# Kernel optimization log

Hardware: AMD Instinct MI355X
Metric: run time of the kernel (lower is better)

Reference implementation:

```python
import jax, jax.numpy as jnp
import numpy as np

N_NODES = 500_000
N_EDGES = 4_000_000


def setup_inputs() -> dict:
    key = jax.random.key(0)
    k1, k2, k3, k4 = jax.random.split(key, 4)
    x = jax.random.normal(k1, (N_NODES, 3), dtype=jnp.float32)
    edge_index = jax.random.randint(k2, (2, N_EDGES), 0, N_NODES, dtype=jnp.int32)
    # GCNConv(3, 16) and GCNConv(16, 1): weight [in, out], bias [out]
    W1 = jax.random.normal(k3, (3, 16), dtype=jnp.float32) / np.sqrt(3.0)
    b1 = jnp.zeros((16,), dtype=jnp.float32)
    W2 = jax.random.normal(k4, (16, 1), dtype=jnp.float32) / np.sqrt(16.0)
    b2 = jnp.zeros((1,), dtype=jnp.float32)
    return {"x": x, "edge_index": edge_index, "W1": W1, "b1": b1, "W2": W2, "b2": b2}


def gcn_conv(x, edge_index, W, b):
    """PyG GCNConv: add self-loops, symmetric deg^-1/2 normalization,
    linear transform, scatter-add aggregation to target nodes, bias."""
    n = x.shape[0]
    loop = jnp.arange(n, dtype=edge_index.dtype)
    row = jnp.concatenate([edge_index[0], loop])  # source nodes
    col = jnp.concatenate([edge_index[1], loop])  # target nodes
    deg = jax.ops.segment_sum(jnp.ones_like(col, dtype=x.dtype), col, num_segments=n)
    deg_inv_sqrt = jnp.where(deg > 0, jax.lax.rsqrt(jnp.maximum(deg, 1.0)), 0.0)
    norm = deg_inv_sqrt[row] * deg_inv_sqrt[col]  # [E+N]
    h = x @ W  # [N, out]
    msg = h[row] * norm[:, None]  # gather + scale, [E+N, out]
    out = jax.ops.segment_sum(msg, col, num_segments=n)  # scatter-add
    return out + b


def reference(x, edge_index, W1, b1, W2, b2):
    h = jax.nn.relu(gcn_conv(x, edge_index, W1, b1))
    return gcn_conv(h, edge_index, W2, b2)  # [N, 1]
```

## Files before the change

### kernel.cpp

```cpp
#include <hip/hip_runtime.h>
#include <hip/hip_fp16.h>


typedef float vf4 __attribute__((ext_vector_type(4)));

#define NB 512
#define SHIFT 10
#define SLICE 1024
#define CAP 11264
#define P1T 1024
#define P1PER 16
#define P1G 256
#define SENT 0xFFFFFFFFu

__global__ __launch_bounds__(1024) void p1_partition(
        const int* __restrict__ row, const int* __restrict__ col,
        unsigned* __restrict__ gcur, unsigned* __restrict__ buf, int E) {
    __shared__ unsigned hist[NB];
    __shared__ unsigned loff[NB], lcur[NB], gbase[NB], bcnt[NB];
    __shared__ unsigned stage[P1T * P1PER];
    __shared__ unsigned wsum[16];
    int t = threadIdx.x;
    if (t < NB) hist[t] = 0;
    __syncthreads();
    int per = (E + P1G - 1) / P1G;
    per = (per + 3) & ~3;
    long long base = (long long)blockIdx.x * per;
    long long eend = base + per; if (eend > E) eend = E;
    int nch = (per + 4095) / 4096;
    unsigned ent[P1PER];
    int bkt[P1PER];
#pragma unroll
    for (int ch = 0; ch < 4; ch++) {
        if (ch < nch) {
            long long e = base + (long long)ch * 4096 + 4 * t;
            if (e + 3 < eend) {
                int4 c4 = *(const int4*)(col + e);
                int4 r4 = *(const int4*)(row + e);
                int cs[4] = {c4.x, c4.y, c4.z, c4.w};
                int rs[4] = {r4.x, r4.y, r4.z, r4.w};
#pragma unroll
                for (int u = 0; u < 4; u++) {
                    int j = ch * 4 + u;
                    ent[j] = ((unsigned)rs[u] << SHIFT) | (unsigned)(cs[u] & (SLICE - 1));
                    bkt[j] = cs[u] >> SHIFT;
                    atomicAdd(&hist[bkt[j]], 1u);
                }
            } else {
#pragma unroll
                for (int u = 0; u < 4; u++) {
                    int j = ch * 4 + u;
                    long long ee = e + u;
                    if (ee < eend) {
                        int c = col[ee], r = row[ee];
                        ent[j] = ((unsigned)r << SHIFT) | (unsigned)(c & (SLICE - 1));
                        bkt[j] = c >> SHIFT;
                        atomicAdd(&hist[bkt[j]], 1u);
                    } else bkt[j] = -1;
                }
            }
        } else {
#pragma unroll
            for (int u = 0; u < 4; u++) bkt[ch * 4 + u] = -1;
        }
    }
    __syncthreads();
    unsigned myc = 0, v = 0;
    int lane = t & 63, w = t >> 6;
    if (t < NB) {
        myc = hist[t];
        v = myc;
#pragma unroll
        for (int d = 1; d < 64; d <<= 1) {
            unsigned o = __shfl_up(v, d, 64);
            if (lane >= d) v += o;
        }
        if (lane == 63) wsum[w] = v;
    }
    __syncthreads();
    if (w == 0) {
        unsigned s = (lane < 8) ? wsum[lane] : 0u, sv = s;
#pragma unroll
        for (int d = 1; d < 8; d <<= 1) {
            unsigned o = __shfl_up(sv, d, 64);
            if (lane >= d) sv += o;
        }
        if (lane < 8) wsum[lane] = sv - s;
    }
    __syncthreads();
    if (t < NB) {
        unsigned excl = v - myc + wsum[w];
        loff[t] = excl;
        lcur[t] = excl;
        bcnt[t] = myc;
        unsigned padded = (myc + 3u) & ~3u;
        gbase[t] = padded ? atomicAdd(&gcur[t], padded) : 0u;
        hist[t] = padded;
    }
    __syncthreads();
#pragma unroll
    for (int j = 0; j < P1PER; j++) {
        if (bkt[j] >= 0) {
            unsigned p = atomicAdd(&lcur[bkt[j]], 1u);
            stage[p] = ent[j];
        }
    }
    __syncthreads();
    for (int bb = 0; bb < 32; bb++) {
        int bk = (w << 5) + bb;
        unsigned c = bcnt[bk], padded = hist[bk];
        unsigned lo = loff[bk], gb = gbase[bk];
        unsigned* dst = buf + (size_t)bk * CAP + gb;
        for (unsigned s = lane; s < padded; s += 64) {
            unsigned val = (s < c) ? stage[lo + s] : SENT;
            if (gb + s < CAP) dst[s] = val;
        }
    }
}

__global__ __launch_bounds__(1024, 8) void k2a1(
        const unsigned* __restrict__ gcur, const unsigned* __restrict__ buf,
        const float* __restrict__ x, uint2* __restrict__ xs4h,
        unsigned* __restrict__ pstart, int N) {
    __shared__ unsigned cnts[SLICE];
    __shared__ unsigned wsum[16];
    int b = blockIdx.x, t = threadIdx.x;
    cnts[t] = 0;
    __syncthreads();
    unsigned ext = min(gcur[b], (unsigned)CAP);
    const unsigned* bp = buf + (size_t)b * CAP;
    for (unsigned i = 4 * t; i < ext; i += 4096) {
        uint4 q = *(const uint4*)(bp + i);
        if (q.x != SENT) atomicAdd(&cnts[q.x & (SLICE - 1)], 1u);
        if (q.y != SENT) atomicAdd(&cnts[q.y & (SLICE - 1)], 1u);
        if (q.z != SENT) atomicAdd(&cnts[q.z & (SLICE - 1)], 1u);
        if (q.w != SENT) atomicAdd(&cnts[q.w & (SLICE - 1)], 1u);
    }
    __syncthreads();
    unsigned myc = cnts[t];
    unsigned pc = (myc + 3u) & ~3u;
    unsigned v = pc;
    int lane = t & 63, w = t >> 6;
#pragma unroll
    for (int d = 1; d < 64; d <<= 1) {
        unsigned o = __shfl_up(v, d, 64);
        if (lane >= d) v += o;
    }
    if (lane == 63) wsum[w] = v;
    __syncthreads();
    if (w == 0) {
        unsigned s = (lane < 16) ? wsum[lane] : 0u, sv = s;
#pragma unroll
        for (int d = 1; d < 16; d <<= 1) {
            unsigned o = __shfl_up(sv, d, 64);
            if (lane >= d) sv += o;
        }
        if (lane < 16) wsum[lane] = sv - s;
    }
    __syncthreads();
    unsigned excl = v - pc + wsum[w];
    int c = (b << SHIFT) + t;
    pstart[c] = (excl << 8) | min(myc, 255u);
    if (c < N) {
        float d = rsqrtf(1.0f + (float)myc);
        __half2 h01 = __floats2half2_rn(d * x[3 * c], d * x[3 * c + 1]);
        __half2 h23 = __floats2half2_rn(d * x[3 * c + 2], 0.f);
        uint2 u;
        u.x = *(unsigned*)&h01;
        u.y = *(unsigned*)&h23;
        xs4h[c] = u;
    }
}

__global__ __launch_bounds__(1024, 8) void k2bf(
        const unsigned* __restrict__ gcur, const unsigned* __restrict__ buf,
        const unsigned* __restrict__ pstart, const uint2* __restrict__ xs4h,
        const float* __restrict__ W1, const float* __restrict__ b1,
        const float* __restrict__ W2, unsigned* __restrict__ buf2,
        float* __restrict__ hs2, int N) {
    __shared__ __align__(16) unsigned sorted[CAP];
    __shared__ unsigned pos[SLICE];
    __shared__ unsigned stot;
    __shared__ float sW[48], sb[16], sw2[16];
    int b = blockIdx.x, t = threadIdx.x;
    if (t < 48) sW[t] = W1[t];
    if (t < 16) { sb[t] = b1[t]; sw2[t] = W2[t]; }
    unsigned meta = pstart[(b << SHIFT) + t];
    pos[t] = meta >> 8;
    if (t == SLICE - 1) {
        unsigned tt = (meta >> 8) + (((meta & 255u) + 3u) & ~3u);
        stot = min(tt, (unsigned)CAP);
    }
    __syncthreads();
    unsigned ext = min(gcur[b], (unsigned)CAP);
    const unsigned* bp = buf + (size_t)b * CAP;
    for (unsigned i = 4 * t; i < ext; i += 4096) {
        uint4 q = *(const uint4*)(bp + i);
        if (q.x != SENT) { unsigned p = atomicAdd(&pos[q.x & (SLICE - 1)], 1u); if (p < CAP) sorted[p] = q.x >> SHIFT; }
        if (q.y != SENT) { unsigned p = atomicAdd(&pos[q.y & (SLICE - 1)], 1u); if (p < CAP) sorted[p] = q.y >> SHIFT; }
        if (q.z != SENT) { unsigned p = atomicAdd(&pos[q.z & (SLICE - 1)], 1u); if (p < CAP) sorted[p] = q.z >> SHIFT; }
        if (q.w != SENT) { unsigned p = atomicAdd(&pos[q.w & (SLICE - 1)], 1u); if (p < CAP) sorted[p] = q.w >> SHIFT; }
    }
    __syncthreads();
    unsigned tot = stot;
    unsigned* b2p = buf2 + (size_t)b * CAP;
    for (unsigned i = 4 * t; i < tot; i += 4096)
        *(uint4*)(b2p + i) = *(const uint4*)(sorted + i);
    int c = (b << SHIFT) + t;
    if (c >= N) return;
    unsigned cnt = meta & 255u;
    unsigned base = meta >> 8;
    float d = rsqrtf(1.0f + (float)cnt);
    uint2 us = xs4h[c];
    float2 fs = __half22float2(*(__half2*)&us.x);
    float a0 = fs.x, a1 = fs.y, a2 = __low2float(*(__half2*)&us.y);
    unsigned j = 0;
    for (; j + 4 <= cnt; j += 4) {
        uint4 rr = *(const uint4*)(sorted + base + j);
        uint2 u0 = xs4h[rr.x], u1 = xs4h[rr.y], u2 = xs4h[rr.z], u3 = xs4h[rr.w];
        float2 f0 = __half22float2(*(__half2*)&u0.x); float g0 = __low2float(*(__half2*)&u0.y);
        float2 f1 = __half22float2(*(__half2*)&u1.x); float g1 = __low2float(*(__half2*)&u1.y);
        float2 f2 = __half22float2(*(__half2*)&u2.x); float g2 = __low2float(*(__half2*)&u2.y);
        float2 f3 = __half22float2(*(__half2*)&u3.x); float g3 = __low2float(*(__half2*)&u3.y);
        a0 += (f0.x + f1.x) + (f2.x + f3.x);
        a1 += (f0.y + f1.y) + (f2.y + f3.y);
        a2 += (g0 + g1) + (g2 + g3);
    }
    for (; j < cnt; j++) {
        uint2 u = xs4h[sorted[base + j]];
        float2 f = __half22float2(*(__half2*)&u.x);
        a0 += f.x; a1 += f.y; a2 += __low2float(*(__half2*)&u.y);
    }
    float s = 0.f;
#pragma unroll
    for (int k = 0; k < 16; k++) {
        float z = fmaxf(d * (a0 * sW[k] + a1 * sW[16 + k] + a2 * sW[32 + k]) + sb[k], 0.f);
        s += z * sw2[k];
    }
    hs2[c] = d * s;
}

__global__ __launch_bounds__(1024, 8) void k2c(
        const unsigned* __restrict__ pstart, const unsigned* __restrict__ buf2,
        const float* __restrict__ hs2, const float* __restrict__ b2,
        float* __restrict__ out, int N) {
    int b = blockIdx.x, t = threadIdx.x;
    int c = (b << SHIFT) + t;
    if (c >= N) return;
    unsigned meta = pstart[c];
    const unsigned* sp = buf2 + (size_t)b * CAP + (meta >> 8);
    unsigned cnt = meta & 255u;
    float d = rsqrtf(1.0f + (float)cnt);
    float s = hs2[c];
    unsigned j = 0;
    for (; j + 8 <= cnt; j += 8) {
        uint4 ra = *(const uint4*)(sp + j);
        uint4 rb = *(const uint4*)(sp + j + 4);
        float v0 = hs2[ra.x], v1 = hs2[ra.y], v2 = hs2[ra.z], v3 = hs2[ra.w];
        float v4 = hs2[rb.x], v5 = hs2[rb.y], v6 = hs2[rb.z], v7 = hs2[rb.w];
        s += ((v0 + v1) + (v2 + v3)) + ((v4 + v5) + (v6 + v7));
    }
    for (; j + 4 <= cnt; j += 4) {
        uint4 rr = *(const uint4*)(sp + j);
        float v0 = hs2[rr.x], v1 = hs2[rr.y], v2 = hs2[rr.z], v3 = hs2[rr.w];
        s += (v0 + v1) + (v2 + v3);
    }
    for (; j < cnt; j++) s += hs2[sp[j]];
    out[c] = d * s + b2[0];
}

__global__ void fb_deg(const int* __restrict__ col, float* __restrict__ deg, int E) {
    int e = blockIdx.x * blockDim.x + threadIdx.x;
    if (e < E) atomicAdd(&deg[col[e]], 1.0f);
}
__global__ void fb_pass_a(const float* __restrict__ x, const float* __restrict__ deg,
                          float* __restrict__ dis, vf4* __restrict__ xs4, int N) {
    int i = blockIdx.x * blockDim.x + threadIdx.x;
    if (i >= N) return;
    float d = rsqrtf(deg[i] + 1.0f);
    dis[i] = d;
    vf4 v; v.x = d * x[3 * i]; v.y = d * x[3 * i + 1]; v.z = d * x[3 * i + 2]; v.w = 0.f;
    xs4[i] = v;
}
__global__ void fb_aggx(const int* __restrict__ ei, const float* __restrict__ xs4,
                        float* __restrict__ accx, int E) {
    int t = blockIdx.x * blockDim.x + threadIdx.x;
    int e = t >> 2, k = t & 3;
    if (e >= E) return;
    int r = ei[e], c = ei[E + e];
    float val = xs4[4 * r + k];
    if (k < 3) atomicAdd(&accx[4 * c + k], val);
}
__global__ void fb_post1(const vf4* __restrict__ accx, const vf4* __restrict__ xs4,
                         const float* __restrict__ dis, const float* __restrict__ W1,
                         const float* __restrict__ b1, const float* __restrict__ W2,
                         float* __restrict__ hs2, int N) {
    __shared__ float sW[48], sb[16], sw2[16];
    if (threadIdx.x < 48) sW[threadIdx.x] = W1[threadIdx.x];
    if (threadIdx.x < 16) { sb[threadIdx.x] = b1[threadIdx.x]; sw2[threadIdx.x] = W2[threadIdx.x]; }
    __syncthreads();
    int i = blockIdx.x * blockDim.x + threadIdx.x;
    if (i >= N) return;
    vf4 a = accx[i], self = xs4[i];
    float a0 = a.x + self.x, a1 = a.y + self.y, a2 = a.z + self.z;
    float d = dis[i], s = 0.f;
#pragma unroll
    for (int k = 0; k < 16; k++) {
        float z = fmaxf(d * (a0 * sW[k] + a1 * sW[16 + k] + a2 * sW[32 + k]) + sb[k], 0.f);
        s += z * sw2[k];
    }
    hs2[i] = d * s;
}
__global__ void fb_agg2(const int* __restrict__ ei, const float* __restrict__ hs2,
                        float* __restrict__ acc2, int E) {
    int e = blockIdx.x * blockDim.x + threadIdx.x;
    if (e >= E) return;
    atomicAdd(&acc2[ei[E + e]], hs2[ei[e]]);
}
__global__ void fb_fin(const float* __restrict__ acc2, const float* __restrict__ hs2,
                       const float* __restrict__ dis, const float* __restrict__ b2,
                       float* __restrict__ out, int N) {
    int i = blockIdx.x * blockDim.x + threadIdx.x;
    if (i < N) out[i] = dis[i] * (acc2[i] + hs2[i]) + b2[0];
}

extern "C" void kernel_launch(void* const* d_in, const int* in_sizes, int n_in,
                              void* d_out, int out_size, void* d_ws, size_t ws_size,
                              hipStream_t stream) {
    const float* x  = (const float*)d_in[0];
    const int*   ei = (const int*)d_in[1];
    const float* W1 = (const float*)d_in[2];
    const float* b1 = (const float*)d_in[3];
    const float* W2 = (const float*)d_in[4];
    const float* b2 = (const float*)d_in[5];
    float* out = (float*)d_out;

    const int N = in_sizes[0] / 3;
    const int E = in_sizes[1] / 2;
    const int* row = ei;
    const int* col = ei + E;

    float* ws = (float*)d_ws;
    size_t need = (size_t)(1024 + 2 * (size_t)NB * CAP + 3 * (size_t)N
                           + (size_t)NB * SLICE) * 4;

    if (ws_size >= need) {
        unsigned* gcur = (unsigned*)ws;
        unsigned* buf  = (unsigned*)ws + 1024;
        unsigned* buf2 = buf + (size_t)NB * CAP;
        uint2* xs4h = (uint2*)(buf2 + (size_t)NB * CAP);
        float* hs2  = (float*)(xs4h + N);
        unsigned* pstart = (unsigned*)(hs2 + N);

        hipMemsetAsync(gcur, 0, 1024 * sizeof(unsigned), stream);
        p1_partition<<<P1G, P1T, 0, stream>>>(row, col, gcur, buf, E);
        k2a1<<<NB, 1024, 0, stream>>>(gcur, buf, x, xs4h, pstart, N);
        k2bf<<<NB, 1024, 0, stream>>>(gcur, buf, pstart, xs4h, W1, b1, W2, buf2, hs2, N);
        k2c<<<NB, 1024, 0, stream>>>(pstart, buf2, hs2, b2, out, N);
    } else {
        float* deg = ws;
        float* dis = ws + (size_t)N;
        vf4*  xs4 = (vf4*)(ws + 2 * (size_t)N);
        float* accx = ws + 6 * (size_t)N;
        float* hs2 = ws + 10 * (size_t)N;
        float* acc2 = ws + 11 * (size_t)N;
        const int B = 256;
        hipMemsetAsync(deg, 0, (size_t)N * sizeof(float), stream);
        hipMemsetAsync(accx, 0, 4 * (size_t)N * sizeof(float), stream);
        hipMemsetAsync(acc2, 0, (size_t)N * sizeof(float), stream);
        fb_deg<<<(E + B - 1) / B, B, 0, stream>>>(col, deg, E);
        fb_pass_a<<<(N + B - 1) / B, B, 0, stream>>>(x, deg, dis, xs4, N);
        long long t4 = (long long)E * 4;
        fb_aggx<<<(int)((t4 + B - 1) / B), B, 0, stream>>>(ei, (const float*)xs4, accx, E);
        fb_post1<<<(N + B - 1) / B, B, 0, stream>>>((const vf4*)accx, xs4, dis, W1, b1, W2, hs2, N);
        fb_agg2<<<(E + B - 1) / B, B, 0, stream>>>(ei, hs2, acc2, E);
        fb_fin<<<(N + B - 1) / B, B, 0, stream>>>(acc2, hs2, dis, b2, out, N);
    }
}
```

Measured before the change: 157.5 us.

## Fuse count and scatter into one sort kernel using atomic-returned ranks

The per-slice histogram kernel and the local counting-sort scatter are merged into one kernel. Each edge's rank comes from the value returned by the histogram atomic, so the scatter needs no second atomic pass, and the bucket buffer is read once per pass inside the same block instead of being reloaded by a separate kernel. The partition kernel likewise reuses ranks from its histogram atomics, dropping the lcur atomics. The aggregation kernel now reads sorted sources from global buf2, which adds a global read in exchange for a smaller shared-memory footprint. Ranks are packed into 8 bits per edge, which assumes per-destination counts stay below 256 and the slice holds at most 3*4096 entries.

```diff
diff --git a/kernel.cpp b/kernel.cpp
--- a/kernel.cpp
+++ b/kernel.cpp
@@ -13,11 +13,23 @@
 #define P1G 256
 #define SENT 0xFFFFFFFFu
 
+#define RANK4(q, rk) do { \
+    if (q.x != SENT) { unsigned r_ = atomicAdd(&cnts[q.x & (SLICE - 1)], 1u); rk |= min(r_, 255u); } \
+    if (q.y != SENT) { unsigned r_ = atomicAdd(&cnts[q.y & (SLICE - 1)], 1u); rk |= min(r_, 255u) << 8; } \
+    if (q.z != SENT) { unsigned r_ = atomicAdd(&cnts[q.z & (SLICE - 1)], 1u); rk |= min(r_, 255u) << 16; } \
+    if (q.w != SENT) { unsigned r_ = atomicAdd(&cnts[q.w & (SLICE - 1)], 1u); rk |= min(r_, 255u) << 24; } } while (0)
+
+#define SCAT4(q, rk) do { \
+    if (q.x != SENT) { unsigned p_ = cnts[q.x & (SLICE - 1)] + (rk & 255u); if (p_ < CAP) sorted[p_] = q.x >> SHIFT; } \
+    if (q.y != SENT) { unsigned p_ = cnts[q.y & (SLICE - 1)] + ((rk >> 8) & 255u); if (p_ < CAP) sorted[p_] = q.y >> SHIFT; } \
+    if (q.z != SENT) { unsigned p_ = cnts[q.z & (SLICE - 1)] + ((rk >> 16) & 255u); if (p_ < CAP) sorted[p_] = q.z >> SHIFT; } \
+    if (q.w != SENT) { unsigned p_ = cnts[q.w & (SLICE - 1)] + ((rk >> 24) & 255u); if (p_ < CAP) sorted[p_] = q.w >> SHIFT; } } while (0)
+
 __global__ __launch_bounds__(1024) void p1_partition(
         const int* __restrict__ row, const int* __restrict__ col,
         unsigned* __restrict__ gcur, unsigned* __restrict__ buf, int E) {
     __shared__ unsigned hist[NB];
-    __shared__ unsigned loff[NB], lcur[NB], gbase[NB], bcnt[NB];
+    __shared__ unsigned loff[NB], gbase[NB], bcnt[NB];
     __shared__ unsigned stage[P1T * P1PER];
     __shared__ unsigned wsum[16];
     int t = threadIdx.x;
@@ -43,8 +55,9 @@
                 for (int u = 0; u < 4; u++) {
                     int j = ch * 4 + u;
                     ent[j] = ((unsigned)rs[u] << SHIFT) | (unsigned)(cs[u] & (SLICE - 1));
-                    bkt[j] = cs[u] >> SHIFT;
-                    atomicAdd(&hist[bkt[j]], 1u);
+                    unsigned bk = (unsigned)cs[u] >> SHIFT;
+                    unsigned r = atomicAdd(&hist[bk], 1u);
+                    bkt[j] = (int)((r << 10) | bk);
                 }
             } else {
 #pragma unroll
@@ -52,10 +65,11 @@
                     int j = ch * 4 + u;
                     long long ee = e + u;
                     if (ee < eend) {
-                        int c = col[ee], r = row[ee];
-                        ent[j] = ((unsigned)r << SHIFT) | (unsigned)(c & (SLICE - 1));
-                        bkt[j] = c >> SHIFT;
-                        atomicAdd(&hist[bkt[j]], 1u);
+                        int c = col[ee], rw = row[ee];
+                        ent[j] = ((unsigned)rw << SHIFT) | (unsigned)(c & (SLICE - 1));
+                        unsigned bk = (unsigned)c >> SHIFT;
+                        unsigned r = atomicAdd(&hist[bk], 1u);
+                        bkt[j] = (int)((r << 10) | bk);
                     } else bkt[j] = -1;
                 }
             }
@@ -91,7 +105,6 @@
     if (t < NB) {
         unsigned excl = v - myc + wsum[w];
         loff[t] = excl;
-        lcur[t] = excl;
         bcnt[t] = myc;
         unsigned padded = (myc + 3u) & ~3u;
         gbase[t] = padded ? atomicAdd(&gcur[t], padded) : 0u;
@@ -101,8 +114,8 @@
 #pragma unroll
     for (int j = 0; j < P1PER; j++) {
         if (bkt[j] >= 0) {
-            unsigned p = atomicAdd(&lcur[bkt[j]], 1u);
-            stage[p] = ent[j];
+            unsigned bb = (unsigned)bkt[j];
+            stage[loff[bb & 1023u] + (bb >> 10)] = ent[j];
         }
     }
     __syncthreads();
@@ -118,23 +131,26 @@
     }
 }
 
-__global__ __launch_bounds__(1024, 8) void k2a1(
+__global__ __launch_bounds__(1024, 8) void k2s(
         const unsigned* __restrict__ gcur, const unsigned* __restrict__ buf,
         const float* __restrict__ x, uint2* __restrict__ xs4h,
-        unsigned* __restrict__ pstart, int N) {
+        unsigned* __restrict__ pstart, unsigned* __restrict__ buf2, int N) {
+    __shared__ __align__(16) unsigned sorted[CAP];
     __shared__ unsigned cnts[SLICE];
     __shared__ unsigned wsum[16];
+    __shared__ unsigned stot;
     int b = blockIdx.x, t = threadIdx.x;
     cnts[t] = 0;
     __syncthreads();
     unsigned ext = min(gcur[b], (unsigned)CAP);
     const unsigned* bp = buf + (size_t)b * CAP;
-    for (unsigned i = 4 * t; i < ext; i += 4096) {
-        uint4 q = *(const uint4*)(bp + i);
-        if (q.x != SENT) atomicAdd(&cnts[q.x & (SLICE - 1)], 1u);
-        if (q.y != SENT) atomicAdd(&cnts[q.y & (SLICE - 1)], 1u);
-        if (q.z != SENT) atomicAdd(&cnts[q.z & (SLICE - 1)], 1u);
-        if (q.w != SENT) atomicAdd(&cnts[q.w & (SLICE - 1)], 1u);
+    unsigned i0 = 4u * (unsigned)t, i1 = i0 + 4096u, i2 = i0 + 8192u;
+    unsigned rk0 = 0, rk1 = 0, rk2 = 0;
+    {
+        uint4 q;
+        if (i0 < ext) { q = *(const uint4*)(bp + i0); RANK4(q, rk0); }
+        if (i1 < ext) { q = *(const uint4*)(bp + i1); RANK4(q, rk1); }
+        if (i2 < ext) { q = *(const uint4*)(bp + i2); RANK4(q, rk2); }
     }
     __syncthreads();
     unsigned myc = cnts[t];
@@ -170,53 +186,44 @@
         u.y = *(unsigned*)&h23;
         xs4h[c] = u;
     }
-}
-
-__global__ __launch_bounds__(1024, 8) void k2bf(
-        const unsigned* __restrict__ gcur, const unsigned* __restrict__ buf,
-        const unsigned* __restrict__ pstart, const uint2* __restrict__ xs4h,
+    cnts[t] = excl;
+    if (t == SLICE - 1) stot = min(excl + pc, (unsigned)CAP);
+    __syncthreads();
+    {
+        uint4 q;
+        if (i0 < ext) { q = *(const uint4*)(bp + i0); SCAT4(q, rk0); }
+        if (i1 < ext) { q = *(const uint4*)(bp + i1); SCAT4(q, rk1); }
+        if (i2 < ext) { q = *(const uint4*)(bp + i2); SCAT4(q, rk2); }
+    }
+    __syncthreads();
+    unsigned tot = stot;
+    unsigned* b2p = buf2 + (size_t)b * CAP;
+    for (unsigned i = 4 * t; i < tot; i += 4096)
+        *(uint4*)(b2p + i) = *(const uint4*)(sorted + i);
+}
+
+__global__ __launch_bounds__(1024, 8) void kC(
+        const unsigned* __restrict__ pstart, const unsigned* __restrict__ buf2,
+        const uint2* __restrict__ xs4h,
         const float* __restrict__ W1, const float* __restrict__ b1,
-        const float* __restrict__ W2, unsigned* __restrict__ buf2,
-        float* __restrict__ hs2, int N) {
-    __shared__ __align__(16) unsigned sorted[CAP];
-    __shared__ unsigned pos[SLICE];
-    __shared__ unsigned stot;
+        const float* __restrict__ W2, float* __restrict__ hs2, int N) {
     __shared__ float sW[48], sb[16], sw2[16];
     int b = blockIdx.x, t = threadIdx.x;
     if (t < 48) sW[t] = W1[t];
     if (t < 16) { sb[t] = b1[t]; sw2[t] = W2[t]; }
-    unsigned meta = pstart[(b << SHIFT) + t];
-    pos[t] = meta >> 8;
-    if (t == SLICE - 1) {
-        unsigned tt = (meta >> 8) + (((meta & 255u) + 3u) & ~3u);
-        stot = min(tt, (unsigned)CAP);
-    }
-    __syncthreads();
-    unsigned ext = min(gcur[b], (unsigned)CAP);
-    const unsigned* bp = buf + (size_t)b * CAP;
-    for (unsigned i = 4 * t; i < ext; i += 4096) {
-        uint4 q = *(const uint4*)(bp + i);
-        if (q.x != SENT) { unsigned p = atomicAdd(&pos[q.x & (SLICE - 1)], 1u); if (p < CAP) sorted[p] = q.x >> SHIFT; }
-        if (q.y != SENT) { unsigned p = atomicAdd(&pos[q.y & (SLICE - 1)], 1u); if (p < CAP) sorted[p] = q.y >> SHIFT; }
-        if (q.z != SENT) { unsigned p = atomicAdd(&pos[q.z & (SLICE - 1)], 1u); if (p < CAP) sorted[p] = q.z >> SHIFT; }
-        if (q.w != SENT) { unsigned p = atomicAdd(&pos[q.w & (SLICE - 1)], 1u); if (p < CAP) sorted[p] = q.w >> SHIFT; }
-    }
-    __syncthreads();
-    unsigned tot = stot;
-    unsigned* b2p = buf2 + (size_t)b * CAP;
-    for (unsigned i = 4 * t; i < tot; i += 4096)
-        *(uint4*)(b2p + i) = *(const uint4*)(sorted + i);
+    __syncthreads();
     int c = (b << SHIFT) + t;
     if (c >= N) return;
+    unsigned meta = pstart[c];
+    const unsigned* sp = buf2 + (size_t)b * CAP + (meta >> 8);
     unsigned cnt = meta & 255u;
-    unsigned base = meta >> 8;
     float d = rsqrtf(1.0f + (float)cnt);
     uint2 us = xs4h[c];
     float2 fs = __half22float2(*(__half2*)&us.x);
     float a0 = fs.x, a1 = fs.y, a2 = __low2float(*(__half2*)&us.y);
     unsigned j = 0;
     for (; j + 4 <= cnt; j += 4) {
-        uint4 rr = *(const uint4*)(sorted + base + j);
+        uint4 rr = *(const uint4*)(sp + j);
         uint2 u0 = xs4h[rr.x], u1 = xs4h[rr.y], u2 = xs4h[rr.z], u3 = xs4h[rr.w];
         float2 f0 = __half22float2(*(__half2*)&u0.x); float g0 = __low2float(*(__half2*)&u0.y);
         float2 f1 = __half22float2(*(__half2*)&u1.x); float g1 = __low2float(*(__half2*)&u1.y);
@@ -227,7 +234,7 @@
         a2 += (g0 + g1) + (g2 + g3);
     }
     for (; j < cnt; j++) {
-        uint2 u = xs4h[sorted[base + j]];
+        uint2 u = xs4h[sp[j]];
         float2 f = __half22float2(*(__half2*)&u.x);
         a0 += f.x; a1 += f.y; a2 += __low2float(*(__half2*)&u.y);
     }
@@ -354,8 +361,8 @@
 
         hipMemsetAsync(gcur, 0, 1024 * sizeof(unsigned), stream);
         p1_partition<<<P1G, P1T, 0, stream>>>(row, col, gcur, buf, E);
-        k2a1<<<NB, 1024, 0, stream>>>(gcur, buf, x, xs4h, pstart, N);
-        k2bf<<<NB, 1024, 0, stream>>>(gcur, buf, pstart, xs4h, W1, b1, W2, buf2, hs2, N);
+        k2s<<<NB, 1024, 0, stream>>>(gcur, buf, x, xs4h, pstart, buf2, N);
+        kC<<<NB, 1024, 0, stream>>>(pstart, buf2, xs4h, W1, b1, W2, hs2, N);
         k2c<<<NB, 1024, 0, stream>>>(pstart, buf2, hs2, b2, out, N);
     } else {
         float* deg = ws;
```

Measured after the change: 168.6 us. 7.1% more time.

## Sort nodes by in-degree within each block to balance gather loops across warps

Applied to the files above, without the earlier changes.

Builds a per-block counting sort of the 1024 nodes by clamped in-degree in k2a1 and writes the metadata into the sorted slot, packing the original cell index alongside offset and count. k2bf and k2c then assign threads to nodes in degree order, so lanes in a wavefront run similar loop trip counts and divergence in the gather loops drops. It costs an extra shared histogram, a scan and several barriers, scatters output writes to hs2 and out, and narrows the offset field to 14 bits.

```diff
diff --git a/kernel.cpp b/kernel.cpp
--- a/kernel.cpp
+++ b/kernel.cpp
@@ -123,9 +123,11 @@
         const float* __restrict__ x, uint2* __restrict__ xs4h,
         unsigned* __restrict__ pstart, int N) {
     __shared__ unsigned cnts[SLICE];
+    __shared__ unsigned h2[256];
     __shared__ unsigned wsum[16];
     int b = blockIdx.x, t = threadIdx.x;
     cnts[t] = 0;
+    if (t < 256) h2[t] = 0;
     __syncthreads();
     unsigned ext = min(gcur[b], (unsigned)CAP);
     const unsigned* bp = buf + (size_t)b * CAP;
@@ -138,6 +140,8 @@
     }
     __syncthreads();
     unsigned myc = cnts[t];
+    unsigned key = min(myc, 255u);
+    unsigned r2 = atomicAdd(&h2[key], 1u);
     unsigned pc = (myc + 3u) & ~3u;
     unsigned v = pc;
     int lane = t & 63, w = t >> 6;
@@ -160,7 +164,6 @@
     __syncthreads();
     unsigned excl = v - pc + wsum[w];
     int c = (b << SHIFT) + t;
-    pstart[c] = (excl << 8) | min(myc, 255u);
     if (c < N) {
         float d = rsqrtf(1.0f + (float)myc);
         __half2 h01 = __floats2half2_rn(d * x[3 * c], d * x[3 * c + 1]);
@@ -170,6 +173,33 @@
         u.y = *(unsigned*)&h23;
         xs4h[c] = u;
     }
+    __syncthreads();
+    unsigned myh = 0, v2 = 0;
+    if (t < 256) {
+        myh = h2[t];
+        v2 = myh;
+#pragma unroll
+        for (int d = 1; d < 64; d <<= 1) {
+            unsigned o = __shfl_up(v2, d, 64);
+            if (lane >= d) v2 += o;
+        }
+        if (lane == 63) wsum[w] = v2;
+    }
+    __syncthreads();
+    if (w == 0) {
+        unsigned s = (lane < 4) ? wsum[lane] : 0u, sv = s;
+#pragma unroll
+        for (int d = 1; d < 4; d <<= 1) {
+            unsigned o = __shfl_up(sv, d, 64);
+            if (lane >= d) sv += o;
+        }
+        if (lane < 4) wsum[lane] = sv - s;
+    }
+    __syncthreads();
+    if (t < 256) h2[t] = v2 - myh + wsum[w];
+    __syncthreads();
+    unsigned spos = h2[key] + r2;
+    pstart[(b << SHIFT) + (int)spos] = (excl << 18) | ((unsigned)t << 8) | key;
 }
 
 __global__ __launch_bounds__(1024, 8) void k2bf(
@@ -186,9 +216,11 @@
     if (t < 48) sW[t] = W1[t];
     if (t < 16) { sb[t] = b1[t]; sw2[t] = W2[t]; }
     unsigned meta = pstart[(b << SHIFT) + t];
-    pos[t] = meta >> 8;
-    if (t == SLICE - 1) {
-        unsigned tt = (meta >> 8) + (((meta & 255u) + 3u) & ~3u);
+    unsigned cell = (meta >> 8) & 1023u;
+    unsigned excl = meta >> 18;
+    pos[cell] = excl;
+    if (cell == SLICE - 1) {
+        unsigned tt = excl + (((meta & 255u) + 3u) & ~3u);
         stot = min(tt, (unsigned)CAP);
     }
     __syncthreads();
@@ -206,38 +238,39 @@
     unsigned* b2p = buf2 + (size_t)b * CAP;
     for (unsigned i = 4 * t; i < tot; i += 4096)
         *(uint4*)(b2p + i) = *(const uint4*)(sorted + i);
-    int c = (b << SHIFT) + t;
-    if (c >= N) return;
-    unsigned cnt = meta & 255u;
-    unsigned base = meta >> 8;
-    float d = rsqrtf(1.0f + (float)cnt);
-    uint2 us = xs4h[c];
-    float2 fs = __half22float2(*(__half2*)&us.x);
-    float a0 = fs.x, a1 = fs.y, a2 = __low2float(*(__half2*)&us.y);
-    unsigned j = 0;
-    for (; j + 4 <= cnt; j += 4) {
-        uint4 rr = *(const uint4*)(sorted + base + j);
-        uint2 u0 = xs4h[rr.x], u1 = xs4h[rr.y], u2 = xs4h[rr.z], u3 = xs4h[rr.w];
-        float2 f0 = __half22float2(*(__half2*)&u0.x); float g0 = __low2float(*(__half2*)&u0.y);
-        float2 f1 = __half22float2(*(__half2*)&u1.x); float g1 = __low2float(*(__half2*)&u1.y);
-        float2 f2 = __half22float2(*(__half2*)&u2.x); float g2 = __low2float(*(__half2*)&u2.y);
-        float2 f3 = __half22float2(*(__half2*)&u3.x); float g3 = __low2float(*(__half2*)&u3.y);
-        a0 += (f0.x + f1.x) + (f2.x + f3.x);
-        a1 += (f0.y + f1.y) + (f2.y + f3.y);
-        a2 += (g0 + g1) + (g2 + g3);
-    }
-    for (; j < cnt; j++) {
-        uint2 u = xs4h[sorted[base + j]];
-        float2 f = __half22float2(*(__half2*)&u.x);
-        a0 += f.x; a1 += f.y; a2 += __low2float(*(__half2*)&u.y);
-    }
-    float s = 0.f;
-#pragma unroll
-    for (int k = 0; k < 16; k++) {
-        float z = fmaxf(d * (a0 * sW[k] + a1 * sW[16 + k] + a2 * sW[32 + k]) + sb[k], 0.f);
-        s += z * sw2[k];
-    }
-    hs2[c] = d * s;
+    int c = (b << SHIFT) + (int)cell;
+    if (c < N) {
+        unsigned cnt = meta & 255u;
+        unsigned base = excl;
+        float d = rsqrtf(1.0f + (float)cnt);
+        uint2 us = xs4h[c];
+        float2 fs = __half22float2(*(__half2*)&us.x);
+        float a0 = fs.x, a1 = fs.y, a2 = __low2float(*(__half2*)&us.y);
+        unsigned j = 0;
+        for (; j + 4 <= cnt; j += 4) {
+            uint4 rr = *(const uint4*)(sorted + base + j);
+            uint2 u0 = xs4h[rr.x], u1 = xs4h[rr.y], u2 = xs4h[rr.z], u3 = xs4h[rr.w];
+            float2 f0 = __half22float2(*(__half2*)&u0.x); float g0 = __low2float(*(__half2*)&u0.y);
+            float2 f1 = __half22float2(*(__half2*)&u1.x); float g1 = __low2float(*(__half2*)&u1.y);
+            float2 f2 = __half22float2(*(__half2*)&u2.x); float g2 = __low2float(*(__half2*)&u2.y);
+            float2 f3 = __half22float2(*(__half2*)&u3.x); float g3 = __low2float(*(__half2*)&u3.y);
+            a0 += (f0.x + f1.x) + (f2.x + f3.x);
+            a1 += (f0.y + f1.y) + (f2.y + f3.y);
+            a2 += (g0 + g1) + (g2 + g3);
+        }
+        for (; j < cnt; j++) {
+            uint2 u = xs4h[sorted[base + j]];
+            float2 f = __half22float2(*(__half2*)&u.x);
+            a0 += f.x; a1 += f.y; a2 += __low2float(*(__half2*)&u.y);
+        }
+        float s = 0.f;
+#pragma unroll
+        for (int k = 0; k < 16; k++) {
+            float z = fmaxf(d * (a0 * sW[k] + a1 * sW[16 + k] + a2 * sW[32 + k]) + sb[k], 0.f);
+            s += z * sw2[k];
+        }
+        hs2[c] = d * s;
+    }
 }
 
 __global__ __launch_bounds__(1024, 8) void k2c(
@@ -245,10 +278,11 @@
         const float* __restrict__ hs2, const float* __restrict__ b2,
         float* __restrict__ out, int N) {
     int b = blockIdx.x, t = threadIdx.x;
-    int c = (b << SHIFT) + t;
+    unsigned meta = pstart[(b << SHIFT) + t];
+    unsigned cell = (meta >> 8) & 1023u;
+    int c = (b << SHIFT) + (int)cell;
     if (c >= N) return;
-    unsigned meta = pstart[c];
-    const unsigned* sp = buf2 + (size_t)b * CAP + (meta >> 8);
+    const unsigned* sp = buf2 + (size_t)b * CAP + (meta >> 18);
     unsigned cnt = meta & 255u;
     float d = rsqrtf(1.0f + (float)cnt);
     float s = hs2[c];
```

New measurement: 163.8 us. 1.04x slower.
